# Kernel tuning notes

Measured on AMD Instinct MI355X. Metric: run time of the kernel, lower is better.

Reference implementation:

```python
import jax, jax.numpy as jnp
from jax import lax
import numpy as np

B, L, C, H, W = 2, 5, 32, 48, 176
NUM_ITER = 1  # args['num_iteration']


def _affine_grid(M, Ho, Wo):
    # torch F.affine_grid, align_corners=False. M: (..., 2, 3) -> (..., Ho, Wo, 2)
    xs = (2.0 * jnp.arange(Wo, dtype=M.dtype) + 1.0) / Wo - 1.0
    ys = (2.0 * jnp.arange(Ho, dtype=M.dtype) + 1.0) / Ho - 1.0
    X, Y = jnp.meshgrid(xs, ys)  # (Ho, Wo)
    base = jnp.stack([X, Y, jnp.ones_like(X)], axis=-1)  # (Ho, Wo, 3)
    return jnp.einsum('...ij,hwj->...hwi', M, base)


def _grid_sample(img, grid):
    # torch F.grid_sample bilinear, zero padding, align_corners=False.
    # img: (C, H, W), grid: (Ho, Wo, 2) normalized coords -> (C, Ho, Wo)
    Ci, Hi, Wi = img.shape
    ix = ((grid[..., 0] + 1.0) * Wi - 1.0) * 0.5
    iy = ((grid[..., 1] + 1.0) * Hi - 1.0) * 0.5
    x0 = jnp.floor(ix)
    y0 = jnp.floor(iy)
    wx = ix - x0
    wy = iy - y0

    def tap(xf, yf):
        valid = ((xf >= 0) & (xf <= Wi - 1) & (yf >= 0) & (yf <= Hi - 1)).astype(img.dtype)
        xi = jnp.clip(xf, 0, Wi - 1).astype(jnp.int32)
        yi = jnp.clip(yf, 0, Hi - 1).astype(jnp.int32)
        return img[:, yi, xi] * valid  # (C, Ho, Wo)

    return (tap(x0, y0) * (1 - wx) * (1 - wy)
            + tap(x0 + 1, y0) * wx * (1 - wy)
            + tap(x0, y0 + 1) * (1 - wx) * wy
            + tap(x0 + 1, y0 + 1) * wx * wy)


_warp_batch = jax.vmap(_grid_sample)


def setup_inputs() -> dict:
    key = jax.random.key(0)
    ks = jax.random.split(key, 6)
    x = jax.random.normal(ks[0], (B * L, C, H, W), dtype=jnp.float32)
    record_len = jnp.full((B,), L, dtype=jnp.int64)
    eye = jnp.array([[1.0, 0.0, 0.0], [0.0, 1.0, 0.0]], dtype=jnp.float32)
    M = eye + 0.1 * jax.random.normal(ks[1], (B, L, L, 2, 3), dtype=jnp.float32)
    msg_w = jax.random.normal(ks[2], (C, 2 * C, 3, 3), dtype=jnp.float32) * (1.0 / np.sqrt(2 * C * 9))
    msg_b = jnp.zeros((C,), dtype=jnp.float32)
    mlp_w = jax.random.normal(ks[3], (C, C), dtype=jnp.float32) * (1.0 / np.sqrt(C))
    mlp_b = jnp.zeros((C,), dtype=jnp.float32)
    return {"x": x, "record_len": record_len, "normalized_affine_matrix": M,
            "msg_w": msg_w, "msg_b": msg_b, "mlp_w": mlp_w, "mlp_b": mlp_b}


def reference(x, record_len, normalized_affine_matrix, msg_w, msg_b, mlp_w, mlp_b):
    M = normalized_affine_matrix
    feat = x.reshape(B, L, C, H, W)  # regroup (record_len == L per batch)

    grids = _affine_grid(M, H, W).reshape(B * L * L, H, W, 2)

    # roi mask: warp an all-ones image with each pairwise transform
    ones_img = jnp.ones((1, H, W), dtype=x.dtype)
    mask = jax.vmap(lambda g: _grid_sample(ones_img, g))(grids)
    mask = mask.reshape(B, L, L, 1, H, W)

    for _ in range(NUM_ITER):
        # warped[b,i,j] = warp(feat[b,j], M[b,i,j])
        imgs = jnp.broadcast_to(feat[:, None], (B, L, L, C, H, W)).reshape(B * L * L, C, H, W)
        warped = _warp_batch(imgs, grids).reshape(B, L, L, C, H, W)
        ego = jnp.broadcast_to(feat[:, :, None], (B, L, L, C, H, W))
        cat = jnp.concatenate([warped, ego], axis=3).reshape(B * L * L, 2 * C, H, W)
        msg = lax.conv_general_dilated(cat, msg_w, (1, 1), ((1, 1), (1, 1)),
                                       dimension_numbers=('NCHW', 'OIHW', 'NCHW'))
        msg = msg + msg_b[None, :, None, None]
        msg = msg.reshape(B, L, L, C, H, W) * mask
        agg = jnp.max(msg, axis=2)  # 'max' agg over neighbors j -> (B, L, C, H, W)
        feat = feat + agg  # gru_flag=False branch

    out = feat[:, 0]  # ego agent feature, (B, C, H, W)
    out = jnp.einsum('bchw,dc->bdhw', out, mlp_w) + mlp_b[None, :, None, None]
    return out
```

## Files before the change

### kernel.cpp

```cpp
#include <hip/hip_runtime.h>
#include <hip/hip_bf16.h>
#include <math.h>

#define BB 2
#define LL 5
#define CC 32
#define HH 48
#define WW 176
#define HWs (HH * WW)
#define BL (BB * LL)

typedef __attribute__((ext_vector_type(8))) short bf16x8;
typedef __attribute__((ext_vector_type(4))) float f32x4;

__device__ __forceinline__ unsigned short f2bf(float v) {
    __hip_bfloat16 h = __float2bfloat16(v);
    return *reinterpret_cast<unsigned short*>(&h);
}

__device__ __forceinline__ void bilin_weights(const float* __restrict__ Mp, int h, int w,
                                              int& o00, int& o10, int& o01, int& o11,
                                              float& a00, float& a10, float& a01, float& a11)
{
    float xs = (2.0f * (float)w + 1.0f) / (float)WW - 1.0f;
    float ys = (2.0f * (float)h + 1.0f) / (float)HH - 1.0f;
    float gx = Mp[0] * xs + Mp[1] * ys + Mp[2];
    float gy = Mp[3] * xs + Mp[4] * ys + Mp[5];
    float ix = ((gx + 1.0f) * (float)WW - 1.0f) * 0.5f;
    float iy = ((gy + 1.0f) * (float)HH - 1.0f) * 0.5f;
    float x0f = floorf(ix), y0f = floorf(iy);
    float wx = ix - x0f, wy = iy - y0f;
    float x1f = x0f + 1.0f, y1f = y0f + 1.0f;
    bool vx0 = (x0f >= 0.0f) && (x0f <= (float)(WW - 1));
    bool vx1 = (x1f >= 0.0f) && (x1f <= (float)(WW - 1));
    bool vy0 = (y0f >= 0.0f) && (y0f <= (float)(HH - 1));
    bool vy1 = (y1f >= 0.0f) && (y1f <= (float)(HH - 1));
    int xi0 = (int)fminf(fmaxf(x0f, 0.0f), (float)(WW - 1));
    int xi1 = (int)fminf(fmaxf(x1f, 0.0f), (float)(WW - 1));
    int yi0 = (int)fminf(fmaxf(y0f, 0.0f), (float)(HH - 1));
    int yi1 = (int)fminf(fmaxf(y1f, 0.0f), (float)(HH - 1));
    o00 = yi0 * WW + xi0;
    o10 = yi0 * WW + xi1;
    o01 = yi1 * WW + xi0;
    o11 = yi1 * WW + xi1;
    a00 = (vx0 && vy0) ? (1.0f - wx) * (1.0f - wy) : 0.0f;
    a10 = (vx1 && vy0) ? wx * (1.0f - wy) : 0.0f;
    a01 = (vx0 && vy1) ? (1.0f - wx) * wy : 0.0f;
    a11 = (vx1 && vy1) ? wx * wy : 0.0f;
}

__global__ __launch_bounds__(256) void k_prep(const float* __restrict__ x,
                                              const float* __restrict__ M,
                                              const float* __restrict__ msg_w,
                                              const float* __restrict__ mlp_w,
                                              unsigned short* __restrict__ warpedcl,
                                              unsigned short* __restrict__ egocl,
                                              float* __restrict__ x0cl,
                                              float* __restrict__ maskb,
                                              unsigned short* __restrict__ Wp,
                                              unsigned short* __restrict__ Wp2)
{
    int y = blockIdx.y;
    if (y < BL) {
        int pix = blockIdx.x * 256 + threadIdx.x;
        int cg  = blockIdx.z;
        int w = pix % WW, h = pix / WW;
        int b = y / LL, j = y % LL;
        const float* Mp = M + (size_t)(b * LL * LL + j) * 6;
        int o00, o10, o01, o11;
        float a00, a10, a01, a11;
        bilin_weights(Mp, h, w, o00, o10, o01, o11, a00, a10, a01, a11);
        if (cg == 0)
            maskb[(size_t)y * HWs + pix] = a00 + a10 + a01 + a11;
        const float* img = x + (size_t)y * CC * HWs + (size_t)cg * 8 * HWs;
        bf16x8 v8;
#pragma unroll
        for (int c = 0; c < 8; ++c) {
            const float* ip = img + (size_t)c * HWs;
            float v = a00 * ip[o00] + a10 * ip[o10] + a01 * ip[o01] + a11 * ip[o11];
            v8[c] = (short)f2bf(v);
        }
        *(bf16x8*)(warpedcl + ((size_t)y * HWs + pix) * CC + cg * 8) = v8;
    } else if (y < BL + BB) {
        int b = y - BL;
        int pix = blockIdx.x * 256 + threadIdx.x;
        int cg  = blockIdx.z;
        const float* img = x + (size_t)(b * LL) * CC * HWs + (size_t)cg * 8 * HWs;
        float v[8];
        bf16x8 v8;
#pragma unroll
        for (int c = 0; c < 8; ++c) {
            v[c] = img[(size_t)c * HWs + pix];
            v8[c] = (short)f2bf(v[c]);
        }
        *(bf16x8*)(egocl + ((size_t)b * HWs + pix) * CC + cg * 8) = v8;
        float* xp = x0cl + ((size_t)b * HWs + pix) * CC + cg * 8;
        *(float4*)xp       = make_float4(v[0], v[1], v[2], v[3]);
        *(float4*)(xp + 4) = make_float4(v[4], v[5], v[6], v[7]);
    } else {
        int i = (blockIdx.z * gridDim.x + blockIdx.x) * 256 + threadIdx.x;
        if (i < 2 * 9 * 32 * 32) {
            int half = i / (9 * 32 * 32);
            int r    = i % (9 * 32 * 32);
            int tap  = r / (32 * 32);
            int r2   = r % (32 * 32);
            int oc   = r2 / 32;
            int ic   = r2 % 32;
            Wp[i] = f2bf(msg_w[(size_t)oc * 576 + (size_t)(half * 32 + ic) * 9 + tap]);
        } else if (i < 2 * 9 * 32 * 32 + 32 * 32) {
            int k = i - 2 * 9 * 32 * 32;
            Wp2[k] = f2bf(mlp_w[k]);
        }
    }
}

__global__ __launch_bounds__(256) void k_fused(const unsigned short* __restrict__ warpedcl,
                                               const unsigned short* __restrict__ egocl,
                                               const float* __restrict__ x0cl,
                                               const float* __restrict__ maskb,
                                               const unsigned short* __restrict__ Wp,
                                               const unsigned short* __restrict__ Wp2,
                                               const float* __restrict__ msg_b,
                                               const float* __restrict__ mlp_b,
                                               float* __restrict__ out)
{
    __shared__ float fl[64][33];
    int wv   = threadIdx.x >> 6;
    int lane = threadIdx.x & 63;
    int lo   = lane & 15;
    int kblk = lane >> 4;
    int b    = blockIdx.y;
    int p0   = blockIdx.x * 64 + wv * 16;
    int pf   = p0 + lo;
    int ph   = pf / WW, pw = pf % WW;

    int ps[9];
    unsigned vbits = 0;
#pragma unroll
    for (int tap = 0; tap < 9; ++tap) {
        int dy = tap / 3 - 1, dx = tap % 3 - 1;
        int hh = ph + dy, wwp = pw + dx;
        bool valid = (hh >= 0) && (hh < HH) && (wwp >= 0) && (wwp < WW);
        ps[tap] = valid ? (pf + dy * WW + dx) : pf;
        vbits |= (valid ? 1u : 0u) << tap;
    }
    const bf16x8 zero = {0, 0, 0, 0, 0, 0, 0, 0};

    bf16x8 Bw[9][2];
#pragma unroll
    for (int tap = 0; tap < 9; ++tap)
#pragma unroll
        for (int nt = 0; nt < 2; ++nt)
            Bw[tap][nt] = *(const bf16x8*)(Wp + ((size_t)(tap * 32 + nt * 16 + lo) * 32 + kblk * 8));

    f32x4 acce[2] = {};
    {
        const unsigned short* Ae = egocl + (size_t)b * HWs * CC;
#pragma unroll
        for (int tap = 0; tap < 9; ++tap) {
            bf16x8 Af = *(const bf16x8*)(Ae + (size_t)ps[tap] * CC + kblk * 8);
            if (!((vbits >> tap) & 1)) Af = zero;
#pragma unroll
            for (int nt = 0; nt < 2; ++nt) {
                bf16x8 Bf = *(const bf16x8*)(Wp + 9 * 32 * 32 + ((size_t)(tap * 32 + nt * 16 + lo) * 32 + kblk * 8));
                acce[nt] = __builtin_amdgcn_mfma_f32_16x16x32_bf16(Af, Bf, acce[nt], 0, 0, 0);
            }
        }
        float b0 = msg_b[lo], b1 = msg_b[16 + lo];
#pragma unroll
        for (int r = 0; r < 4; ++r) { acce[0][r] += b0; acce[1][r] += b1; }
    }

    f32x4 agg[2];
#pragma unroll
    for (int r = 0; r < 4; ++r) { agg[0][r] = -INFINITY; agg[1][r] = -INFINITY; }

    for (int j = 0; j < LL; ++j) {
        const unsigned short* Aw = warpedcl + (size_t)(b * LL + j) * HWs * CC;
        f32x4 acc[2] = {};
#pragma unroll
        for (int tap = 0; tap < 9; ++tap) {
            bf16x8 Af = *(const bf16x8*)(Aw + (size_t)ps[tap] * CC + kblk * 8);
            if (!((vbits >> tap) & 1)) Af = zero;
#pragma unroll
            for (int nt = 0; nt < 2; ++nt)
                acc[nt] = __builtin_amdgcn_mfma_f32_16x16x32_bf16(Af, Bw[tap][nt], acc[nt], 0, 0, 0);
        }
        float4 mk = *(const float4*)(maskb + (size_t)(b * LL + j) * HWs + p0 + kblk * 4);
        float mkr[4] = {mk.x, mk.y, mk.z, mk.w};
#pragma unroll
        for (int nt = 0; nt < 2; ++nt)
#pragma unroll
            for (int r = 0; r < 4; ++r)
                agg[nt][r] = fmaxf(agg[nt][r], (acc[nt][r] + acce[nt][r]) * mkr[r]);
    }

#pragma unroll
    for (int nt = 0; nt < 2; ++nt)
#pragma unroll
        for (int r = 0; r < 4; ++r) {
            int pixl = kblk * 4 + r;
            float f = agg[nt][r] + x0cl[((size_t)b * HWs + p0 + pixl) * CC + nt * 16 + lo];
            fl[wv * 16 + pixl][nt * 16 + lo] = f;
        }

    bf16x8 Afm;
#pragma unroll
    for (int e = 0; e < 8; ++e)
        Afm[e] = (short)f2bf(fl[wv * 16 + lo][kblk * 8 + e]);

#pragma unroll
    for (int nt2 = 0; nt2 < 2; ++nt2) {
        bf16x8 Bm = *(const bf16x8*)(Wp2 + ((size_t)(nt2 * 16 + lo) * 32 + kblk * 8));
        f32x4 om = {};
        om = __builtin_amdgcn_mfma_f32_16x16x32_bf16(Afm, Bm, om, 0, 0, 0);
        float mb2 = mlp_b[nt2 * 16 + lo];
        int d = nt2 * 16 + lo;
#pragma unroll
        for (int r = 0; r < 4; ++r)
            out[((size_t)b * CC + d) * HWs + p0 + kblk * 4 + r] = om[r] + mb2;
    }
}

extern "C" void kernel_launch(void* const* d_in, const int* in_sizes, int n_in,
                              void* d_out, int out_size, void* d_ws, size_t ws_size,
                              hipStream_t stream)
{
    (void)in_sizes; (void)n_in; (void)out_size; (void)ws_size;
    const float* x     = (const float*)d_in[0];
    const float* M     = (const float*)d_in[2];
    const float* msg_w = (const float*)d_in[3];
    const float* msg_b = (const float*)d_in[4];
    const float* mlp_w = (const float*)d_in[5];
    const float* mlp_b = (const float*)d_in[6];
    float* out = (float*)d_out;

    unsigned short* Wp       = (unsigned short*)d_ws;
    unsigned short* Wp2      = Wp + 2 * 9 * 32 * 32;
    unsigned short* warpedcl = Wp2 + 32 * 32;
    unsigned short* egocl    = warpedcl + (size_t)BL * HWs * CC;
    float*          x0cl     = (float*)(egocl + (size_t)BB * HWs * CC);
    float*          maskb    = x0cl + (size_t)BB * HWs * CC;

    {
        dim3 g(HWs / 256, BL + BB + 1, 4);
        k_prep<<<g, 256, 0, stream>>>(x, M, msg_w, mlp_w,
                                      warpedcl, egocl, x0cl, maskb, Wp, Wp2);
    }
    {
        dim3 g(HWs / 64, BB);
        k_fused<<<g, 256, 0, stream>>>(warpedcl, egocl, x0cl, maskb, Wp, Wp2,
                                       msg_b, mlp_b, out);
    }
}
```

Measured before the change: 30.42 us.

## Fuse warp, conv, max-aggregate and MLP into one tiled warp-specialized kernel

Replaces the two-kernel pipeline, which went through global memory, with a single kernel over 8x8 spatial tiles. Each block stages the ego tile and the bilinear-warped neighbor tiles (with halo) in shared memory, and converts the weights to bf16 in LDS. Producer waves warp the next neighbor into a double buffer while consumer waves run the MFMA conv on the current one. This removes the global round-trip of the warped/ego/mask intermediates and one launch. In exchange, every block redoes the weight conversion and the halo warping, and it adds barriers per neighbor. The skip connection now reads the bf16 ego copy instead of the fp32 input, which lowers precision.

```diff
diff --git a/kernel.cpp b/kernel.cpp
--- a/kernel.cpp
+++ b/kernel.cpp
@@ -8,7 +8,13 @@
 #define HH 48
 #define WW 176
 #define HWs (HH * WW)
-#define BL (BB * LL)
+
+#define TR 8
+#define TC 8
+#define HR 10
+#define HC 10
+#define PXS 40
+#define IMG_ELE (HR * HC * PXS)
 
 typedef __attribute__((ext_vector_type(8))) short bf16x8;
 typedef __attribute__((ext_vector_type(4))) float f32x4;
@@ -16,6 +22,10 @@
 __device__ __forceinline__ unsigned short f2bf(float v) {
     __hip_bfloat16 h = __float2bfloat16(v);
     return *reinterpret_cast<unsigned short*>(&h);
+}
+__device__ __forceinline__ float bf2f(unsigned short u) {
+    __hip_bfloat16 h = *reinterpret_cast<__hip_bfloat16*>(&u);
+    return __bfloat162float(h);
 }
 
 __device__ __forceinline__ void bilin_weights(const float* __restrict__ Mp, int h, int w,
@@ -49,176 +59,172 @@
     a11 = (vx1 && vy1) ? wx * wy : 0.0f;
 }
 
-__global__ __launch_bounds__(256) void k_prep(const float* __restrict__ x,
-                                              const float* __restrict__ M,
-                                              const float* __restrict__ msg_w,
-                                              const float* __restrict__ mlp_w,
-                                              unsigned short* __restrict__ warpedcl,
-                                              unsigned short* __restrict__ egocl,
-                                              float* __restrict__ x0cl,
-                                              float* __restrict__ maskb,
-                                              unsigned short* __restrict__ Wp,
-                                              unsigned short* __restrict__ Wp2)
-{
-    int y = blockIdx.y;
-    if (y < BL) {
-        int pix = blockIdx.x * 256 + threadIdx.x;
-        int cg  = blockIdx.z;
-        int w = pix % WW, h = pix / WW;
-        int b = y / LL, j = y % LL;
-        const float* Mp = M + (size_t)(b * LL * LL + j) * 6;
+__device__ __forceinline__ void stage_unit(const float* __restrict__ x,
+                                           const float* __restrict__ Mp,
+                                           int b, int j, int u, int r0, int c0,
+                                           unsigned short* __restrict__ dst,
+                                           float* __restrict__ maskrow)
+{
+    int px = u >> 2, cg = u & 3;
+    int hr = px / HC, hc = px % HC;
+    int gr = r0 + hr - 1, gc = c0 + hc - 1;
+    unsigned short* dp = dst + px * PXS + cg * 8;
+    if (gr < 0 || gr >= HH || gc < 0 || gc >= WW) {
+        const bf16x8 z = {0, 0, 0, 0, 0, 0, 0, 0};
+        *(bf16x8*)dp = z;
+        return;
+    }
+    bf16x8 v8;
+    if (j < 0) {
+        const float* ip = x + ((size_t)(b * LL) * CC + cg * 8) * HWs + gr * WW + gc;
+#pragma unroll
+        for (int c = 0; c < 8; ++c)
+            v8[c] = (short)f2bf(ip[(size_t)c * HWs]);
+    } else {
         int o00, o10, o01, o11;
         float a00, a10, a01, a11;
-        bilin_weights(Mp, h, w, o00, o10, o01, o11, a00, a10, a01, a11);
-        if (cg == 0)
-            maskb[(size_t)y * HWs + pix] = a00 + a10 + a01 + a11;
-        const float* img = x + (size_t)y * CC * HWs + (size_t)cg * 8 * HWs;
-        bf16x8 v8;
+        bilin_weights(Mp, gr, gc, o00, o10, o01, o11, a00, a10, a01, a11);
+        if (cg == 0 && hr >= 1 && hr <= TR && hc >= 1 && hc <= TC)
+            maskrow[(hr - 1) * TC + (hc - 1)] = a00 + a10 + a01 + a11;
+        const float* ip = x + ((size_t)(b * LL + j) * CC + cg * 8) * HWs;
 #pragma unroll
         for (int c = 0; c < 8; ++c) {
-            const float* ip = img + (size_t)c * HWs;
-            float v = a00 * ip[o00] + a10 * ip[o10] + a01 * ip[o01] + a11 * ip[o11];
-            v8[c] = (short)f2bf(v);
-        }
-        *(bf16x8*)(warpedcl + ((size_t)y * HWs + pix) * CC + cg * 8) = v8;
-    } else if (y < BL + BB) {
-        int b = y - BL;
-        int pix = blockIdx.x * 256 + threadIdx.x;
-        int cg  = blockIdx.z;
-        const float* img = x + (size_t)(b * LL) * CC * HWs + (size_t)cg * 8 * HWs;
-        float v[8];
-        bf16x8 v8;
-#pragma unroll
-        for (int c = 0; c < 8; ++c) {
-            v[c] = img[(size_t)c * HWs + pix];
-            v8[c] = (short)f2bf(v[c]);
-        }
-        *(bf16x8*)(egocl + ((size_t)b * HWs + pix) * CC + cg * 8) = v8;
-        float* xp = x0cl + ((size_t)b * HWs + pix) * CC + cg * 8;
-        *(float4*)xp       = make_float4(v[0], v[1], v[2], v[3]);
-        *(float4*)(xp + 4) = make_float4(v[4], v[5], v[6], v[7]);
-    } else {
-        int i = (blockIdx.z * gridDim.x + blockIdx.x) * 256 + threadIdx.x;
-        if (i < 2 * 9 * 32 * 32) {
-            int half = i / (9 * 32 * 32);
-            int r    = i % (9 * 32 * 32);
-            int tap  = r / (32 * 32);
-            int r2   = r % (32 * 32);
-            int oc   = r2 / 32;
-            int ic   = r2 % 32;
-            Wp[i] = f2bf(msg_w[(size_t)oc * 576 + (size_t)(half * 32 + ic) * 9 + tap]);
-        } else if (i < 2 * 9 * 32 * 32 + 32 * 32) {
-            int k = i - 2 * 9 * 32 * 32;
-            Wp2[k] = f2bf(mlp_w[k]);
-        }
-    }
-}
-
-__global__ __launch_bounds__(256) void k_fused(const unsigned short* __restrict__ warpedcl,
-                                               const unsigned short* __restrict__ egocl,
-                                               const float* __restrict__ x0cl,
-                                               const float* __restrict__ maskb,
-                                               const unsigned short* __restrict__ Wp,
-                                               const unsigned short* __restrict__ Wp2,
-                                               const float* __restrict__ msg_b,
-                                               const float* __restrict__ mlp_b,
-                                               float* __restrict__ out)
-{
-    __shared__ float fl[64][33];
-    int wv   = threadIdx.x >> 6;
-    int lane = threadIdx.x & 63;
-    int lo   = lane & 15;
-    int kblk = lane >> 4;
-    int b    = blockIdx.y;
-    int p0   = blockIdx.x * 64 + wv * 16;
-    int pf   = p0 + lo;
-    int ph   = pf / WW, pw = pf % WW;
-
-    int ps[9];
-    unsigned vbits = 0;
-#pragma unroll
-    for (int tap = 0; tap < 9; ++tap) {
-        int dy = tap / 3 - 1, dx = tap % 3 - 1;
-        int hh = ph + dy, wwp = pw + dx;
-        bool valid = (hh >= 0) && (hh < HH) && (wwp >= 0) && (wwp < WW);
-        ps[tap] = valid ? (pf + dy * WW + dx) : pf;
-        vbits |= (valid ? 1u : 0u) << tap;
-    }
-    const bf16x8 zero = {0, 0, 0, 0, 0, 0, 0, 0};
-
-    bf16x8 Bw[9][2];
-#pragma unroll
-    for (int tap = 0; tap < 9; ++tap)
+            const float* q = ip + (size_t)c * HWs;
+            v8[c] = (short)f2bf(a00 * q[o00] + a10 * q[o10] + a01 * q[o01] + a11 * q[o11]);
+        }
+    }
+    *(bf16x8*)dp = v8;
+}
+
+__global__ __launch_bounds__(512) void k_all(const float* __restrict__ x,
+                                             const float* __restrict__ M,
+                                             const float* __restrict__ msg_w,
+                                             const float* __restrict__ msg_b,
+                                             const float* __restrict__ mlp_w,
+                                             const float* __restrict__ mlp_b,
+                                             float* __restrict__ out)
+{
+    __shared__ unsigned short wmsg[2 * 9 * 32 * PXS];
+    __shared__ unsigned short wmlp[32 * PXS];
+    __shared__ unsigned short ego[IMG_ELE];
+    __shared__ unsigned short jbuf[2 * IMG_ELE];
+    __shared__ float maskl[LL][TR * TC];
+
+    const int tid = threadIdx.x;
+    const int b  = blockIdx.z;
+    const int r0 = blockIdx.y * TR;
+    const int c0 = blockIdx.x * TC;
+    const float* Mb = M + (size_t)b * LL * LL * 6;
+
+    for (int i = tid; i < 2 * 9 * 32 * 32; i += 512) {
+        int half = i / (9 * 32 * 32), r = i % (9 * 32 * 32);
+        int tap = r / 1024, r2 = r & 1023, oc = r2 >> 5, ic = r2 & 31;
+        wmsg[((half * 9 + tap) * 32 + oc) * PXS + ic] =
+            f2bf(msg_w[(size_t)oc * 576 + (size_t)(half * 32 + ic) * 9 + tap]);
+    }
+    for (int i = tid; i < 32 * 32; i += 512)
+        wmlp[(i >> 5) * PXS + (i & 31)] = f2bf(mlp_w[i]);
+
+    for (int u = tid; u < 800; u += 512) {
+        if (u < 400) stage_unit(x, nullptr, b, -1, u, r0, c0, ego, nullptr);
+        else         stage_unit(x, Mb, b, 0, u - 400, r0, c0, jbuf, maskl[0]);
+    }
+    __syncthreads();
+
+    const int wv   = tid >> 6;
+    const int lane = tid & 63;
+    const int lo   = lane & 15;
+    const int kblk = lane >> 4;
+    const bool isconv = (wv < 4);
+
+    f32x4 acce[2] = {};
+    f32x4 agg[2];
+#pragma unroll
+    for (int r = 0; r < 4; ++r) { agg[0][r] = -INFINITY; agg[1][r] = -INFINITY; }
+
+    for (int j = 0; j < LL; ++j) {
+        if (!isconv) {
+            if (j < 4) {
+                unsigned short* dstb = jbuf + ((j + 1) & 1) * IMG_ELE;
+                const float* Mp = Mb + (size_t)(j + 1) * 6;
+                for (int u = tid - 256; u < 400; u += 256)
+                    stage_unit(x, Mp, b, j + 1, u, r0, c0, dstb, maskl[j + 1]);
+            }
+        } else {
+            if (j == 0) {
+#pragma unroll
+                for (int tap = 0; tap < 9; ++tap) {
+                    int dy = tap / 3 - 1, dx = tap % 3 - 1;
+                    int hp = (1 + 2 * wv + (lo >> 3) + dy) * HC + (1 + (lo & 7) + dx);
+                    bf16x8 Af = *(const bf16x8*)(ego + hp * PXS + kblk * 8);
+#pragma unroll
+                    for (int nt = 0; nt < 2; ++nt) {
+                        bf16x8 Bf = *(const bf16x8*)(wmsg + (size_t)((9 + tap) * 32 + nt * 16 + lo) * PXS + kblk * 8);
+                        acce[nt] = __builtin_amdgcn_mfma_f32_16x16x32_bf16(Af, Bf, acce[nt], 0, 0, 0);
+                    }
+                }
+                float b0 = msg_b[lo], b1 = msg_b[16 + lo];
+#pragma unroll
+                for (int r = 0; r < 4; ++r) { acce[0][r] += b0; acce[1][r] += b1; }
+            }
+            const unsigned short* jb = jbuf + (j & 1) * IMG_ELE;
+            f32x4 acc[2] = {};
+#pragma unroll
+            for (int tap = 0; tap < 9; ++tap) {
+                int dy = tap / 3 - 1, dx = tap % 3 - 1;
+                int hp = (1 + 2 * wv + (lo >> 3) + dy) * HC + (1 + (lo & 7) + dx);
+                bf16x8 Af = *(const bf16x8*)(jb + hp * PXS + kblk * 8);
+#pragma unroll
+                for (int nt = 0; nt < 2; ++nt) {
+                    bf16x8 Bf = *(const bf16x8*)(wmsg + (size_t)(tap * 32 + nt * 16 + lo) * PXS + kblk * 8);
+                    acc[nt] = __builtin_amdgcn_mfma_f32_16x16x32_bf16(Af, Bf, acc[nt], 0, 0, 0);
+                }
+            }
+            f32x4 mk = *(const f32x4*)&maskl[j][wv * 16 + kblk * 4];
+#pragma unroll
+            for (int nt = 0; nt < 2; ++nt)
+#pragma unroll
+                for (int r = 0; r < 4; ++r)
+                    agg[nt][r] = fmaxf(agg[nt][r], (acc[nt][r] + acce[nt][r]) * mk[r]);
+        }
+        if (j < 4) __syncthreads();
+    }
+    __syncthreads();
+
+    if (isconv) {
+        float* fl = ((float*)jbuf) + wv * (16 * PXS);
 #pragma unroll
         for (int nt = 0; nt < 2; ++nt)
-            Bw[tap][nt] = *(const bf16x8*)(Wp + ((size_t)(tap * 32 + nt * 16 + lo) * 32 + kblk * 8));
-
-    f32x4 acce[2] = {};
-    {
-        const unsigned short* Ae = egocl + (size_t)b * HWs * CC;
-#pragma unroll
-        for (int tap = 0; tap < 9; ++tap) {
-            bf16x8 Af = *(const bf16x8*)(Ae + (size_t)ps[tap] * CC + kblk * 8);
-            if (!((vbits >> tap) & 1)) Af = zero;
-#pragma unroll
-            for (int nt = 0; nt < 2; ++nt) {
-                bf16x8 Bf = *(const bf16x8*)(Wp + 9 * 32 * 32 + ((size_t)(tap * 32 + nt * 16 + lo) * 32 + kblk * 8));
-                acce[nt] = __builtin_amdgcn_mfma_f32_16x16x32_bf16(Af, Bf, acce[nt], 0, 0, 0);
-            }
-        }
-        float b0 = msg_b[lo], b1 = msg_b[16 + lo];
-#pragma unroll
-        for (int r = 0; r < 4; ++r) { acce[0][r] += b0; acce[1][r] += b1; }
-    }
-
-    f32x4 agg[2];
-#pragma unroll
-    for (int r = 0; r < 4; ++r) { agg[0][r] = -INFINITY; agg[1][r] = -INFINITY; }
-
-    for (int j = 0; j < LL; ++j) {
-        const unsigned short* Aw = warpedcl + (size_t)(b * LL + j) * HWs * CC;
-        f32x4 acc[2] = {};
-#pragma unroll
-        for (int tap = 0; tap < 9; ++tap) {
-            bf16x8 Af = *(const bf16x8*)(Aw + (size_t)ps[tap] * CC + kblk * 8);
-            if (!((vbits >> tap) & 1)) Af = zero;
-#pragma unroll
-            for (int nt = 0; nt < 2; ++nt)
-                acc[nt] = __builtin_amdgcn_mfma_f32_16x16x32_bf16(Af, Bw[tap][nt], acc[nt], 0, 0, 0);
-        }
-        float4 mk = *(const float4*)(maskb + (size_t)(b * LL + j) * HWs + p0 + kblk * 4);
-        float mkr[4] = {mk.x, mk.y, mk.z, mk.w};
-#pragma unroll
-        for (int nt = 0; nt < 2; ++nt)
-#pragma unroll
-            for (int r = 0; r < 4; ++r)
-                agg[nt][r] = fmaxf(agg[nt][r], (acc[nt][r] + acce[nt][r]) * mkr[r]);
-    }
-
-#pragma unroll
-    for (int nt = 0; nt < 2; ++nt)
-#pragma unroll
-        for (int r = 0; r < 4; ++r) {
-            int pixl = kblk * 4 + r;
-            float f = agg[nt][r] + x0cl[((size_t)b * HWs + p0 + pixl) * CC + nt * 16 + lo];
-            fl[wv * 16 + pixl][nt * 16 + lo] = f;
-        }
-
-    bf16x8 Afm;
-#pragma unroll
-    for (int e = 0; e < 8; ++e)
-        Afm[e] = (short)f2bf(fl[wv * 16 + lo][kblk * 8 + e]);
-
-#pragma unroll
-    for (int nt2 = 0; nt2 < 2; ++nt2) {
-        bf16x8 Bm = *(const bf16x8*)(Wp2 + ((size_t)(nt2 * 16 + lo) * 32 + kblk * 8));
-        f32x4 om = {};
-        om = __builtin_amdgcn_mfma_f32_16x16x32_bf16(Afm, Bm, om, 0, 0, 0);
-        float mb2 = mlp_b[nt2 * 16 + lo];
-        int d = nt2 * 16 + lo;
-#pragma unroll
-        for (int r = 0; r < 4; ++r)
-            out[((size_t)b * CC + d) * HWs + p0 + kblk * 4 + r] = om[r] + mb2;
+#pragma unroll
+            for (int r = 0; r < 4; ++r) {
+                int m = kblk * 4 + r;
+                int hp = (1 + 2 * wv + (m >> 3)) * HC + 1 + (m & 7);
+                float skip = bf2f(ego[hp * PXS + nt * 16 + lo]);
+                fl[m * PXS + nt * 16 + lo] = agg[nt][r] + skip;
+            }
+        f32x4 q0 = *(const f32x4*)&fl[lo * PXS + kblk * 8];
+        f32x4 q1 = *(const f32x4*)&fl[lo * PXS + kblk * 8 + 4];
+        bf16x8 Afm;
+#pragma unroll
+        for (int e = 0; e < 4; ++e) {
+            Afm[e]     = (short)f2bf(q0[e]);
+            Afm[4 + e] = (short)f2bf(q1[e]);
+        }
+#pragma unroll
+        for (int nt2 = 0; nt2 < 2; ++nt2) {
+            bf16x8 Bm = *(const bf16x8*)(wmlp + (size_t)(nt2 * 16 + lo) * PXS + kblk * 8);
+            f32x4 om = {};
+            om = __builtin_amdgcn_mfma_f32_16x16x32_bf16(Afm, Bm, om, 0, 0, 0);
+            float mb2 = mlp_b[nt2 * 16 + lo];
+            int d = nt2 * 16 + lo;
+#pragma unroll
+            for (int r = 0; r < 4; ++r) {
+                int m = kblk * 4 + r;
+                int gr = r0 + 2 * wv + (m >> 3);
+                int gc = c0 + (m & 7);
+                out[((size_t)(b * CC + d)) * HWs + gr * WW + gc] = om[r] + mb2;
+            }
+        }
     }
 }
 
@@ -226,7 +232,7 @@
                               void* d_out, int out_size, void* d_ws, size_t ws_size,
                               hipStream_t stream)
 {
-    (void)in_sizes; (void)n_in; (void)out_size; (void)ws_size;
+    (void)in_sizes; (void)n_in; (void)out_size; (void)d_ws; (void)ws_size;
     const float* x     = (const float*)d_in[0];
     const float* M     = (const float*)d_in[2];
     const float* msg_w = (const float*)d_in[3];
@@ -235,21 +241,6 @@
     const float* mlp_b = (const float*)d_in[6];
     float* out = (float*)d_out;
 
-    unsigned short* Wp       = (unsigned short*)d_ws;
-    unsigned short* Wp2      = Wp + 2 * 9 * 32 * 32;
-    unsigned short* warpedcl = Wp2 + 32 * 32;
-    unsigned short* egocl    = warpedcl + (size_t)BL * HWs * CC;
-    float*          x0cl     = (float*)(egocl + (size_t)BB * HWs * CC);
-    float*          maskb    = x0cl + (size_t)BB * HWs * CC;
-
-    {
-        dim3 g(HWs / 256, BL + BB + 1, 4);
-        k_prep<<<g, 256, 0, stream>>>(x, M, msg_w, mlp_w,
-                                      warpedcl, egocl, x0cl, maskb, Wp, Wp2);
-    }
-    {
-        dim3 g(HWs / 64, BB);
-        k_fused<<<g, 256, 0, stream>>>(warpedcl, egocl, x0cl, maskb, Wp, Wp2,
-                                       msg_b, mlp_b, out);
-    }
-}
+    dim3 g(WW / TC, HH / TR, BB);
+    k_all<<<g, 512, 0, stream>>>(x, M, msg_w, msg_b, mlp_w, mlp_b, out);
+}
```

Result: slower. 37.52 us (+23.3%).

## Split output channels across waves, prefetch neighbor fragments, drop fp32 skip copy

Applied to the files above, without the earlier changes.

The fused conv kernel now uses 512-thread blocks where each wave computes one 16-channel half of the output, and it prefetches the next neighbor's A fragments into a double buffer while the current neighbor's MFMAs run. The fp32 channel-last copy of the input is removed, and the residual is read from the bf16 ego buffer instead, which cuts workspace writes and reads in the prep kernel. The final MLP output is written with float4 stores. In exchange, the skip connection loses precision relative to fp32, register pressure rises from the prefetch buffers, and a block-wide barrier is added before the MLP stage.

```diff
diff --git a/kernel.cpp b/kernel.cpp
--- a/kernel.cpp
+++ b/kernel.cpp
@@ -16,6 +16,10 @@
 __device__ __forceinline__ unsigned short f2bf(float v) {
     __hip_bfloat16 h = __float2bfloat16(v);
     return *reinterpret_cast<unsigned short*>(&h);
+}
+__device__ __forceinline__ float bf2f(unsigned short u) {
+    __hip_bfloat16 h = *reinterpret_cast<__hip_bfloat16*>(&u);
+    return __bfloat162float(h);
 }
 
 __device__ __forceinline__ void bilin_weights(const float* __restrict__ Mp, int h, int w,
@@ -55,7 +59,6 @@
                                               const float* __restrict__ mlp_w,
                                               unsigned short* __restrict__ warpedcl,
                                               unsigned short* __restrict__ egocl,
-                                              float* __restrict__ x0cl,
                                               float* __restrict__ maskb,
                                               unsigned short* __restrict__ Wp,
                                               unsigned short* __restrict__ Wp2)
@@ -86,17 +89,11 @@
         int pix = blockIdx.x * 256 + threadIdx.x;
         int cg  = blockIdx.z;
         const float* img = x + (size_t)(b * LL) * CC * HWs + (size_t)cg * 8 * HWs;
-        float v[8];
         bf16x8 v8;
 #pragma unroll
-        for (int c = 0; c < 8; ++c) {
-            v[c] = img[(size_t)c * HWs + pix];
-            v8[c] = (short)f2bf(v[c]);
-        }
+        for (int c = 0; c < 8; ++c)
+            v8[c] = (short)f2bf(img[(size_t)c * HWs + pix]);
         *(bf16x8*)(egocl + ((size_t)b * HWs + pix) * CC + cg * 8) = v8;
-        float* xp = x0cl + ((size_t)b * HWs + pix) * CC + cg * 8;
-        *(float4*)xp       = make_float4(v[0], v[1], v[2], v[3]);
-        *(float4*)(xp + 4) = make_float4(v[4], v[5], v[6], v[7]);
     } else {
         int i = (blockIdx.z * gridDim.x + blockIdx.x) * 256 + threadIdx.x;
         if (i < 2 * 9 * 32 * 32) {
@@ -114,9 +111,8 @@
     }
 }
 
-__global__ __launch_bounds__(256) void k_fused(const unsigned short* __restrict__ warpedcl,
+__global__ __launch_bounds__(512) void k_fused(const unsigned short* __restrict__ warpedcl,
                                                const unsigned short* __restrict__ egocl,
-                                               const float* __restrict__ x0cl,
                                                const float* __restrict__ maskb,
                                                const unsigned short* __restrict__ Wp,
                                                const unsigned short* __restrict__ Wp2,
@@ -124,102 +120,107 @@
                                                const float* __restrict__ mlp_b,
                                                float* __restrict__ out)
 {
-    __shared__ float fl[64][33];
-    int wv   = threadIdx.x >> 6;
-    int lane = threadIdx.x & 63;
-    int lo   = lane & 15;
-    int kblk = lane >> 4;
-    int b    = blockIdx.y;
-    int p0   = blockIdx.x * 64 + wv * 16;
-    int pf   = p0 + lo;
-    int ph   = pf / WW, pw = pf % WW;
+    __shared__ float flds[64][36];
+
+    const int tid  = threadIdx.x;
+    const int wv   = tid >> 6;
+    const int lane = tid & 63;
+    const int lo   = lane & 15;
+    const int kblk = lane >> 4;
+    const int nt   = wv >> 2;
+    const int tw   = wv & 3;
+    const int b    = blockIdx.y;
+    const int p0   = blockIdx.x * 64 + tw * 16;
+    const int pf   = p0 + lo;
+    const int ph   = pf / WW, pw = pf % WW;
 
     int ps[9];
     unsigned vbits = 0;
 #pragma unroll
     for (int tap = 0; tap < 9; ++tap) {
         int dy = tap / 3 - 1, dx = tap % 3 - 1;
-        int hh = ph + dy, wwp = pw + dx;
-        bool valid = (hh >= 0) && (hh < HH) && (wwp >= 0) && (wwp < WW);
+        int hh = ph + dy, wq = pw + dx;
+        bool valid = (hh >= 0) && (hh < HH) && (wq >= 0) && (wq < WW);
         ps[tap] = valid ? (pf + dy * WW + dx) : pf;
         vbits |= (valid ? 1u : 0u) << tap;
     }
     const bf16x8 zero = {0, 0, 0, 0, 0, 0, 0, 0};
 
-    bf16x8 Bw[9][2];
+    bf16x8 Bw[9];
 #pragma unroll
     for (int tap = 0; tap < 9; ++tap)
-#pragma unroll
-        for (int nt = 0; nt < 2; ++nt)
-            Bw[tap][nt] = *(const bf16x8*)(Wp + ((size_t)(tap * 32 + nt * 16 + lo) * 32 + kblk * 8));
-
-    f32x4 acce[2] = {};
+        Bw[tap] = *(const bf16x8*)(Wp + ((size_t)(tap * 32 + nt * 16 + lo)) * 32 + kblk * 8);
+
+    bf16x8 afA[9], afB[9];
+    const unsigned short* Ae  = egocl + (size_t)b * HWs * CC;
+    const unsigned short* Aw0 = warpedcl + (size_t)(b * LL) * HWs * CC;
+#pragma unroll
+    for (int tap = 0; tap < 9; ++tap)
+        afA[tap] = *(const bf16x8*)(Ae + (size_t)ps[tap] * CC + kblk * 8);
+#pragma unroll
+    for (int tap = 0; tap < 9; ++tap)
+        afB[tap] = *(const bf16x8*)(Aw0 + (size_t)ps[tap] * CC + kblk * 8);
+
+    f32x4 acce = {};
+#pragma unroll
+    for (int tap = 0; tap < 9; ++tap) {
+        bf16x8 a = ((vbits >> tap) & 1) ? afA[tap] : zero;
+        bf16x8 Be = *(const bf16x8*)(Wp + 9 * 32 * 32 + ((size_t)(tap * 32 + nt * 16 + lo)) * 32 + kblk * 8);
+        acce = __builtin_amdgcn_mfma_f32_16x16x32_bf16(a, Be, acce, 0, 0, 0);
+    }
     {
-        const unsigned short* Ae = egocl + (size_t)b * HWs * CC;
+        float cb = msg_b[nt * 16 + lo];
+#pragma unroll
+        for (int r = 0; r < 4; ++r) acce[r] += cb;
+    }
+
+    f32x4 agg;
+#pragma unroll
+    for (int r = 0; r < 4; ++r) agg[r] = -INFINITY;
+
+#pragma unroll
+    for (int j = 0; j < LL; ++j) {
+        bf16x8* cur = (j & 1) ? afA : afB;
+        bf16x8* nxt = (j & 1) ? afB : afA;
+        if (j < 4) {
+            const unsigned short* Awn = warpedcl + (size_t)(b * LL + j + 1) * HWs * CC;
+#pragma unroll
+            for (int tap = 0; tap < 9; ++tap)
+                nxt[tap] = *(const bf16x8*)(Awn + (size_t)ps[tap] * CC + kblk * 8);
+        }
+        f32x4 acc = {};
 #pragma unroll
         for (int tap = 0; tap < 9; ++tap) {
-            bf16x8 Af = *(const bf16x8*)(Ae + (size_t)ps[tap] * CC + kblk * 8);
-            if (!((vbits >> tap) & 1)) Af = zero;
-#pragma unroll
-            for (int nt = 0; nt < 2; ++nt) {
-                bf16x8 Bf = *(const bf16x8*)(Wp + 9 * 32 * 32 + ((size_t)(tap * 32 + nt * 16 + lo) * 32 + kblk * 8));
-                acce[nt] = __builtin_amdgcn_mfma_f32_16x16x32_bf16(Af, Bf, acce[nt], 0, 0, 0);
-            }
-        }
-        float b0 = msg_b[lo], b1 = msg_b[16 + lo];
-#pragma unroll
-        for (int r = 0; r < 4; ++r) { acce[0][r] += b0; acce[1][r] += b1; }
-    }
-
-    f32x4 agg[2];
-#pragma unroll
-    for (int r = 0; r < 4; ++r) { agg[0][r] = -INFINITY; agg[1][r] = -INFINITY; }
-
-    for (int j = 0; j < LL; ++j) {
-        const unsigned short* Aw = warpedcl + (size_t)(b * LL + j) * HWs * CC;
-        f32x4 acc[2] = {};
-#pragma unroll
-        for (int tap = 0; tap < 9; ++tap) {
-            bf16x8 Af = *(const bf16x8*)(Aw + (size_t)ps[tap] * CC + kblk * 8);
-            if (!((vbits >> tap) & 1)) Af = zero;
-#pragma unroll
-            for (int nt = 0; nt < 2; ++nt)
-                acc[nt] = __builtin_amdgcn_mfma_f32_16x16x32_bf16(Af, Bw[tap][nt], acc[nt], 0, 0, 0);
+            bf16x8 a = ((vbits >> tap) & 1) ? cur[tap] : zero;
+            acc = __builtin_amdgcn_mfma_f32_16x16x32_bf16(a, Bw[tap], acc, 0, 0, 0);
         }
         float4 mk = *(const float4*)(maskb + (size_t)(b * LL + j) * HWs + p0 + kblk * 4);
         float mkr[4] = {mk.x, mk.y, mk.z, mk.w};
 #pragma unroll
-        for (int nt = 0; nt < 2; ++nt)
-#pragma unroll
-            for (int r = 0; r < 4; ++r)
-                agg[nt][r] = fmaxf(agg[nt][r], (acc[nt][r] + acce[nt][r]) * mkr[r]);
-    }
-
-#pragma unroll
-    for (int nt = 0; nt < 2; ++nt)
-#pragma unroll
-        for (int r = 0; r < 4; ++r) {
-            int pixl = kblk * 4 + r;
-            float f = agg[nt][r] + x0cl[((size_t)b * HWs + p0 + pixl) * CC + nt * 16 + lo];
-            fl[wv * 16 + pixl][nt * 16 + lo] = f;
-        }
+        for (int r = 0; r < 4; ++r)
+            agg[r] = fmaxf(agg[r], (acc[r] + acce[r]) * mkr[r]);
+    }
+
+#pragma unroll
+    for (int r = 0; r < 4; ++r) {
+        int px = kblk * 4 + r;
+        float skip = bf2f(egocl[((size_t)b * HWs + p0 + px) * CC + nt * 16 + lo]);
+        flds[tw * 16 + px][nt * 16 + lo] = agg[r] + skip;
+    }
+    __syncthreads();
 
     bf16x8 Afm;
 #pragma unroll
     for (int e = 0; e < 8; ++e)
-        Afm[e] = (short)f2bf(fl[wv * 16 + lo][kblk * 8 + e]);
-
-#pragma unroll
-    for (int nt2 = 0; nt2 < 2; ++nt2) {
-        bf16x8 Bm = *(const bf16x8*)(Wp2 + ((size_t)(nt2 * 16 + lo) * 32 + kblk * 8));
-        f32x4 om = {};
-        om = __builtin_amdgcn_mfma_f32_16x16x32_bf16(Afm, Bm, om, 0, 0, 0);
-        float mb2 = mlp_b[nt2 * 16 + lo];
-        int d = nt2 * 16 + lo;
-#pragma unroll
-        for (int r = 0; r < 4; ++r)
-            out[((size_t)b * CC + d) * HWs + p0 + kblk * 4 + r] = om[r] + mb2;
-    }
+        Afm[e] = (short)f2bf(flds[tw * 16 + lo][kblk * 8 + e]);
+
+    bf16x8 Bm = *(const bf16x8*)(Wp2 + (size_t)(nt * 16 + lo) * 32 + kblk * 8);
+    f32x4 om = {};
+    om = __builtin_amdgcn_mfma_f32_16x16x32_bf16(Afm, Bm, om, 0, 0, 0);
+    float mb2 = mlp_b[nt * 16 + lo];
+    int d = nt * 16 + lo;
+    float4 o4 = make_float4(om[0] + mb2, om[1] + mb2, om[2] + mb2, om[3] + mb2);
+    *(float4*)(out + ((size_t)(b * CC + d)) * HWs + p0 + kblk * 4) = o4;
 }
 
 extern "C" void kernel_launch(void* const* d_in, const int* in_sizes, int n_in,
@@ -239,17 +240,16 @@
     unsigned short* Wp2      = Wp + 2 * 9 * 32 * 32;
     unsigned short* warpedcl = Wp2 + 32 * 32;
     unsigned short* egocl    = warpedcl + (size_t)BL * HWs * CC;
-    float*          x0cl     = (float*)(egocl + (size_t)BB * HWs * CC);
-    float*          maskb    = x0cl + (size_t)BB * HWs * CC;
+    float*          maskb    = (float*)(egocl + (size_t)BB * HWs * CC);
 
     {
         dim3 g(HWs / 256, BL + BB + 1, 4);
         k_prep<<<g, 256, 0, stream>>>(x, M, msg_w, mlp_w,
-                                      warpedcl, egocl, x0cl, maskb, Wp, Wp2);
+                                      warpedcl, egocl, maskb, Wp, Wp2);
     }
     {
         dim3 g(HWs / 64, BB);
-        k_fused<<<g, 256, 0, stream>>>(warpedcl, egocl, x0cl, maskb, Wp, Wp2,
+        k_fused<<<g, 512, 0, stream>>>(warpedcl, egocl, maskb, Wp, Wp2,
                                        msg_b, mlp_b, out);
     }
 }
```

Result: slower. 36.48 us (+19.9%).
